# Kernel optimization log

Measured on AMD Instinct MI355X. Metric: run time of the kernel, lower is better.

The kernel has to match this reference:

```python
import jax, jax.numpy as jnp
from jax import lax
import numpy as np

B, C_IN, C_OUT, H, W = 16, 64, 64, 160, 160
K, STRIDE, PAD, DIL, SHIFT = 3, 1, 1, 1, 1


def setup_inputs() -> dict:
    key = jax.random.key(0)
    kx, kw = jax.random.split(key)
    x = jax.random.normal(kx, (B, C_IN, H, W), dtype=jnp.float32)
    weight = jax.random.normal(kw, (C_OUT, C_IN, K, K), dtype=jnp.float32)
    return {"x": x, "weight": weight}


def reference(x, weight):
    Bn, C, Hh, Ww = x.shape
    # zero-pad spatially by shift_distance on all sides (matches F.pad)
    xp = jnp.pad(x, ((0, 0), (0, 0), (SHIFT, SHIFT), (SHIFT, SHIFT)))
    Hp, Wp = Hh + 2 * SHIFT, Ww + 2 * SHIFT
    # shifts list: (dx, dy) for channel groups c % 5
    dxs = jnp.array([0, SHIFT, 0, -SHIFT, 0])
    dys = jnp.array([0, 0, SHIFT, 0, -SHIFT])
    cmod = jnp.arange(C) % 5
    dy = dys[cmod]  # [C] roll along H (dim 2)
    dx = dxs[cmod]  # [C] roll along W (dim 3)
    # torch.roll semantics: out[h, w] = in[(h - dy) % Hp, (w - dx) % Wp]
    row = (jnp.arange(Hp)[None, :] - dy[:, None]) % Hp  # [C, Hp]
    col = (jnp.arange(Wp)[None, :] - dx[:, None]) % Wp  # [C, Wp]
    # single fused gather over channel-dependent row/col indices
    x_shifted = xp[:, jnp.arange(C)[:, None, None], row[:, :, None], col[:, None, :]]
    out = lax.conv_general_dilated(
        x_shifted, weight,
        window_strides=(STRIDE, STRIDE),
        padding=((PAD, PAD), (PAD, PAD)),
        rhs_dilation=(DIL, DIL),
        dimension_numbers=("NCHW", "OIHW", "NCHW"),
    )
    # crop the extra border introduced by the pre-pad
    return out[:, :, 1:-1, 1:-1]
```

## Files before the change

### kernel.cpp

```cpp
#include <hip/hip_runtime.h>
#include <hip/hip_bf16.h>

#define BATCH 16
#define CIN 64
#define COUT 64
#define HH 160
#define WW 160
#define HP 162
#define WP 162

#define ABUF 21760

typedef __attribute__((ext_vector_type(8))) __bf16 bf16x8;
typedef __attribute__((ext_vector_type(4))) float f32x4;
typedef __attribute__((ext_vector_type(8))) unsigned short ushort8;

typedef __attribute__((address_space(1))) const unsigned int gu32;
typedef __attribute__((address_space(3))) unsigned int lu32;

__global__ __launch_bounds__(256) void prep(const float* __restrict__ x,
                                            const float* __restrict__ w,
                                            unsigned short* __restrict__ xs,
                                            unsigned short* __restrict__ wb) {
  __shared__ float lds[64 * 160];

  if (blockIdx.x >= BATCH * HP) {
    int e = (blockIdx.x - BATCH * HP) * 256 + threadIdx.x;
    if (e < 9 * 64 * 64) {
      int tap = e >> 12;
      int o = (e >> 6) & 63;
      int c = e & 63;
      float v = w[((size_t)(o * 64 + c)) * 9 + tap];
      __hip_bfloat16 h = __float2bfloat16(v);
      wb[e] = *reinterpret_cast<unsigned short*>(&h);
    }
    return;
  }

  int y = blockIdx.x % HP;
  int b = blockIdx.x / HP;
  int tid = threadIdx.x;

#pragma unroll
  for (int it = 0; it < 10; ++it) {
    int idx = it * 256 + tid;
    int c = idx / 40;
    int j = idx - c * 40;
    int cm = c % 5;
    int dx = (cm == 1) ? 1 : ((cm == 3) ? -1 : 0);
    int dy = (cm == 2) ? 1 : ((cm == 4) ? -1 : 0);
    int yy = y - dy;
    f32x4 v = {0.f, 0.f, 0.f, 0.f};
    if (yy >= 1 && yy <= HH)
      v = *reinterpret_cast<const f32x4*>(
          x + (((size_t)(b * CIN + c)) * HH + (size_t)(yy - 1)) * WW + j * 4);
    int rot = (c & 31) + dx;
    if (rot < 0) rot += 160;
    int p0 = 4 * j + rot;
#pragma unroll
    for (int e = 0; e < 4; ++e) {
      int p = p0 + e;
      if (p >= 160) p -= 160;
      lds[c * 160 + p] = v[e];
    }
  }
  __syncthreads();

  int cg = tid & 7;
  int xr = tid >> 3;
  int dxe[8], rote[8], rowb[8];
#pragma unroll
  for (int e = 0; e < 8; ++e) {
    int c = cg * 8 + e;
    int cm = c % 5;
    int dx = (cm == 1) ? 1 : ((cm == 3) ? -1 : 0);
    int rot = (c & 31) + dx;
    if (rot < 0) rot += 160;
    dxe[e] = dx;
    rote[e] = rot;
    rowb[e] = c * 160;
  }
  size_t obase = ((size_t)(b * HP + y) * WP) * CIN + cg * 8;
#pragma unroll
  for (int it = 0; it < 6; ++it) {
    int xi = it * 32 + xr;
    if (xi < WP) {
      ushort8 val;
#pragma unroll
      for (int e = 0; e < 8; ++e) {
        int xx = xi - dxe[e] - 1;
        float v = 0.f;
        if (xx >= 0 && xx < WW) {
          int p = rote[e] + xx;
          if (p >= 160) p -= 160;
          v = lds[rowb[e] + p];
        }
        __hip_bfloat16 h = __float2bfloat16(v);
        val[e] = *reinterpret_cast<unsigned short*>(&h);
      }
      *reinterpret_cast<ushort8*>(xs + obase + (size_t)xi * CIN) = val;
    }
  }
}

__global__ __launch_bounds__(256, 1) void conv_mfma(const unsigned short* __restrict__ xs,
                                                    const unsigned short* __restrict__ wb,
                                                    float* __restrict__ out) {
  __shared__ __align__(16) unsigned short lds_a[ABUF];
  __shared__ __align__(16) unsigned short lds_b[ABUF];
  __shared__ __align__(16) unsigned short lds_w[9 * 64 * 64];

  int tid = threadIdx.x;
  int blk = blockIdx.x;
  int tile0 = (blk & 7) * 32 + (blk >> 3);
  int ntiles = (tile0 < 64) ? 7 : 6;

  int wv = tid >> 6;
  int lane = tid & 63;
  int l15 = lane & 15;
  int q = lane >> 4;

  int goff[11];
#pragma unroll
  for (int r = 0; r < 11; ++r) {
    int u = r * 256 + tid;
    int p = u >> 3;
    int j = (u & 7) ^ (p & 7);
    int pr = p / 34, pc = p - pr * 34;
    goff[r] = (pr * WP + pc) * CIN + j * 8;
  }

  int bw0 = l15 * 64 + ((q ^ (l15 & 7)) * 8);
  int bw1 = l15 * 64 + (((4 + q) ^ (l15 & 7)) * 8);

#define STAGE_TO(BUFARR, T_)                                                   \
  {                                                                            \
    int sb_ = (T_) / 100;                                                      \
    int srr_ = (T_) - sb_ * 100;                                               \
    int sti_ = srr_ / 5, stj_ = srr_ - sti_ * 5;                               \
    const unsigned short* srcb_ = xs +                                         \
        ((size_t)sb_ * HP + (size_t)(sti_ * 8)) * WP * CIN +                   \
        (size_t)(stj_ * 32) * CIN;                                             \
    unsigned short* dst0_ = (BUFARR) + wv * 512;                               \
    _Pragma("unroll") for (int r = 0; r < 10; ++r)                             \
        __builtin_amdgcn_global_load_lds((gu32*)(srcb_ + goff[r]),             \
                                         (lu32*)(dst0_ + r * 2048), 16, 0, 0); \
    if (tid < 160)                                                             \
      __builtin_amdgcn_global_load_lds((gu32*)(srcb_ + goff[10]),              \
                                       (lu32*)(dst0_ + 10 * 2048), 16, 0, 0);  \
  }

#define LOAD_A(RBUF, bufp, tt)                                                 \
  {                                                                            \
    const int ch_ = (tt) / 9, ky_ = ((tt) % 9) / 3, kx_ = (tt) % 3;            \
    _Pragma("unroll") for (int mt = 0; mt < 4; ++mt) {                         \
      int pix = 2 * wv * 34 + l15 +                                            \
                (((mt >> 1) + ky_) * 34 + kx_ + (mt & 1) * 16);                \
      int chunk = (ch_ * 4 + q) ^ (pix & 7);                                   \
      Ab[bufp][mt] =                                                           \
          *reinterpret_cast<const bf16x8*>(&(RBUF)[pix * 64 + chunk * 8]);     \
    }                                                                          \
  }

#define LOAD_BW(bufp, tt)                                                      \
  {                                                                            \
    const int ch_ = (tt) / 9, tap_ = (tt) % 9;                                 \
    _Pragma("unroll") for (int nt = 0; nt < 4; ++nt)                           \
        Bb[bufp][nt] = *reinterpret_cast<const bf16x8*>(                       \
            &lds_w[tap_ * 4096 + nt * 1024 + (ch_ ? bw1 : bw0)]);              \
  }

#define TILE_BODY(I_, RBUF, WBUF)                                              \
  {                                                                            \
    int t_ = tile0 + 256 * (I_);                                               \
    int b_ = t_ / 100;                                                         \
    int rr_ = t_ - b_ * 100;                                                   \
    int ti_ = rr_ / 5, tj_ = rr_ - ti_ * 5;                                    \
    int y0_ = ti_ * 8, x0_ = tj_ * 32;                                         \
    if ((I_) + 1 < ntiles) STAGE_TO(WBUF, tile0 + 256 * ((I_) + 1));           \
    _Pragma("unroll") for (int a_ = 0; a_ < 4; ++a_)                           \
      _Pragma("unroll") for (int c2_ = 0; c2_ < 4; ++c2_)                      \
        acc[a_][c2_] = (f32x4){0.f, 0.f, 0.f, 0.f};                            \
    LOAD_A(RBUF, 0, 0);                                                        \
    LOAD_BW(0, 0);                                                             \
    _Pragma("unroll") for (int tt = 0; tt < 18; ++tt) {                        \
      if (tt + 1 < 18) {                                                       \
        LOAD_A(RBUF, (tt + 1) & 1, tt + 1);                                    \
        LOAD_BW((tt + 1) & 1, tt + 1);                                         \
      }                                                                        \
      _Pragma("unroll") for (int mt = 0; mt < 4; ++mt)                         \
        _Pragma("unroll") for (int nt = 0; nt < 4; ++nt)                       \
          acc[mt][nt] = __builtin_amdgcn_mfma_f32_16x16x32_bf16(               \
              Ab[tt & 1][mt], Bb[tt & 1][nt], acc[mt][nt], 0, 0, 0);           \
    }                                                                          \
    __syncthreads();                                                           \
    _Pragma("unroll") for (int mt = 0; mt < 4; ++mt) {                         \
      int orow_ = y0_ + 2 * wv + (mt >> 1);                                    \
      int xo_ = x0_ + (mt & 1) * 16 + q * 4;                                   \
      _Pragma("unroll") for (int nt = 0; nt < 4; ++nt) {                       \
        int o_ = nt * 16 + l15;                                                \
        *reinterpret_cast<f32x4*>(                                             \
            out + ((size_t)(b_ * COUT + o_) * HH + (size_t)orow_) * WW + xo_) = \
            acc[mt][nt];                                                       \
      }                                                                        \
    }                                                                          \
  }

  f32x4 acc[4][4];
  bf16x8 Ab[2][4];
  bf16x8 Bb[2][4];

  for (int r = 0; r < 18; ++r) {
    int u = r * 256 + tid;
    int orow = u >> 3;
    int jj = (u & 7) ^ (orow & 7);
    __builtin_amdgcn_global_load_lds((gu32*)(wb + orow * 64 + jj * 8),
                                     (lu32*)(lds_w + (u & ~63) * 8), 16, 0, 0);
  }
  STAGE_TO(lds_a, tile0);
  __syncthreads();

  for (int i = 0; i < ntiles; i += 2) {
    TILE_BODY(i, lds_a, lds_b);
    if (i + 1 < ntiles) TILE_BODY(i + 1, lds_b, lds_a);
  }

#undef TILE_BODY
#undef LOAD_BW
#undef LOAD_A
#undef STAGE_TO
}

extern "C" void kernel_launch(void* const* d_in, const int* in_sizes, int n_in,
                              void* d_out, int out_size, void* d_ws, size_t ws_size,
                              hipStream_t stream) {
  const float* x = (const float*)d_in[0];
  const float* w = (const float*)d_in[1];
  float* out = (float*)d_out;

  unsigned short* xs = (unsigned short*)d_ws;
  unsigned short* wb = (unsigned short*)((char*)d_ws + (size_t)BATCH * HP * WP * CIN * 2);

  hipLaunchKernelGGL(prep, dim3(BATCH * HP + 144), dim3(256), 0, stream, x, w, xs, wb);
  hipLaunchKernelGGL(conv_mfma, dim3(256), dim3(256), 0, stream, xs, wb, out);
}
```

Measured before the change: 226.5 us.

## Split conv work across eight waves and simplify shift-staging LDS layout

The conv kernel moves from 256 to 512 threads per block. Each of the eight waves now computes one output row (2 M-tiles) instead of two rows (4 M-tiles), and the staging and weight-load loops are re-indexed to match. s_setprio is raised around the MFMA bursts. The aim is more waves in flight per CU to hide LDS and global latency, at the cost of each wave re-reading the full B fragments, which adds LDS read traffic per MFMA. Separately, the prep kernel drops the rotated LDS placement in favour of a plain row stride of 161 floats, which removes the wraparound index arithmetic while still staggering banks.

After: 232.0 us. +2.4%, slower.

```diff
diff --git a/kernel.cpp b/kernel.cpp
--- a/kernel.cpp
+++ b/kernel.cpp
@@ -10,6 +10,7 @@
 #define WP 162
 
 #define ABUF 21760
+#define PSTR 161
 
 typedef __attribute__((ext_vector_type(8))) __bf16 bf16x8;
 typedef __attribute__((ext_vector_type(4))) float f32x4;
@@ -22,7 +23,7 @@
                                             const float* __restrict__ w,
                                             unsigned short* __restrict__ xs,
                                             unsigned short* __restrict__ wb) {
-  __shared__ float lds[64 * 160];
+  __shared__ float lds[64 * PSTR];
 
   if (blockIdx.x >= BATCH * HP) {
     int e = (blockIdx.x - BATCH * HP) * 256 + threadIdx.x;
@@ -47,38 +48,27 @@
     int c = idx / 40;
     int j = idx - c * 40;
     int cm = c % 5;
-    int dx = (cm == 1) ? 1 : ((cm == 3) ? -1 : 0);
     int dy = (cm == 2) ? 1 : ((cm == 4) ? -1 : 0);
     int yy = y - dy;
     f32x4 v = {0.f, 0.f, 0.f, 0.f};
     if (yy >= 1 && yy <= HH)
       v = *reinterpret_cast<const f32x4*>(
           x + (((size_t)(b * CIN + c)) * HH + (size_t)(yy - 1)) * WW + j * 4);
-    int rot = (c & 31) + dx;
-    if (rot < 0) rot += 160;
-    int p0 = 4 * j + rot;
-#pragma unroll
-    for (int e = 0; e < 4; ++e) {
-      int p = p0 + e;
-      if (p >= 160) p -= 160;
-      lds[c * 160 + p] = v[e];
-    }
+    int p0 = c * PSTR + 4 * j;
+#pragma unroll
+    for (int e = 0; e < 4; ++e) lds[p0 + e] = v[e];
   }
   __syncthreads();
 
   int cg = tid & 7;
   int xr = tid >> 3;
-  int dxe[8], rote[8], rowb[8];
+  int dxe[8], rowb[8];
 #pragma unroll
   for (int e = 0; e < 8; ++e) {
     int c = cg * 8 + e;
     int cm = c % 5;
-    int dx = (cm == 1) ? 1 : ((cm == 3) ? -1 : 0);
-    int rot = (c & 31) + dx;
-    if (rot < 0) rot += 160;
-    dxe[e] = dx;
-    rote[e] = rot;
-    rowb[e] = c * 160;
+    dxe[e] = (cm == 1) ? 1 : ((cm == 3) ? -1 : 0);
+    rowb[e] = c * PSTR;
   }
   size_t obase = ((size_t)(b * HP + y) * WP) * CIN + cg * 8;
 #pragma unroll
@@ -90,11 +80,7 @@
       for (int e = 0; e < 8; ++e) {
         int xx = xi - dxe[e] - 1;
         float v = 0.f;
-        if (xx >= 0 && xx < WW) {
-          int p = rote[e] + xx;
-          if (p >= 160) p -= 160;
-          v = lds[rowb[e] + p];
-        }
+        if (xx >= 0 && xx < WW) v = lds[rowb[e] + xx];
         __hip_bfloat16 h = __float2bfloat16(v);
         val[e] = *reinterpret_cast<unsigned short*>(&h);
       }
@@ -103,7 +89,7 @@
   }
 }
 
-__global__ __launch_bounds__(256, 1) void conv_mfma(const unsigned short* __restrict__ xs,
+__global__ __launch_bounds__(512, 1) void conv_mfma(const unsigned short* __restrict__ xs,
                                                     const unsigned short* __restrict__ wb,
                                                     float* __restrict__ out) {
   __shared__ __align__(16) unsigned short lds_a[ABUF];
@@ -120,10 +106,10 @@
   int l15 = lane & 15;
   int q = lane >> 4;
 
-  int goff[11];
-#pragma unroll
-  for (int r = 0; r < 11; ++r) {
-    int u = r * 256 + tid;
+  int goff[6];
+#pragma unroll
+  for (int r = 0; r < 6; ++r) {
+    int u = r * 512 + tid;
     int p = u >> 3;
     int j = (u & 7) ^ (p & 7);
     int pr = p / 34, pc = p - pr * 34;
@@ -142,20 +128,19 @@
         ((size_t)sb_ * HP + (size_t)(sti_ * 8)) * WP * CIN +                   \
         (size_t)(stj_ * 32) * CIN;                                             \
     unsigned short* dst0_ = (BUFARR) + wv * 512;                               \
-    _Pragma("unroll") for (int r = 0; r < 10; ++r)                             \
+    _Pragma("unroll") for (int r = 0; r < 5; ++r)                              \
         __builtin_amdgcn_global_load_lds((gu32*)(srcb_ + goff[r]),             \
-                                         (lu32*)(dst0_ + r * 2048), 16, 0, 0); \
+                                         (lu32*)(dst0_ + r * 4096), 16, 0, 0); \
     if (tid < 160)                                                             \
-      __builtin_amdgcn_global_load_lds((gu32*)(srcb_ + goff[10]),              \
-                                       (lu32*)(dst0_ + 10 * 2048), 16, 0, 0);  \
+      __builtin_amdgcn_global_load_lds((gu32*)(srcb_ + goff[5]),               \
+                                       (lu32*)(dst0_ + 5 * 4096), 16, 0, 0);   \
   }
 
 #define LOAD_A(RBUF, bufp, tt)                                                 \
   {                                                                            \
     const int ch_ = (tt) / 9, ky_ = ((tt) % 9) / 3, kx_ = (tt) % 3;            \
-    _Pragma("unroll") for (int mt = 0; mt < 4; ++mt) {                         \
-      int pix = 2 * wv * 34 + l15 +                                            \
-                (((mt >> 1) + ky_) * 34 + kx_ + (mt & 1) * 16);                \
+    _Pragma("unroll") for (int mt = 0; mt < 2; ++mt) {                         \
+      int pix = (wv + ky_) * 34 + kx_ + l15 + mt * 16;                         \
       int chunk = (ch_ * 4 + q) ^ (pix & 7);                                   \
       Ab[bufp][mt] =                                                           \
           *reinterpret_cast<const bf16x8*>(&(RBUF)[pix * 64 + chunk * 8]);     \
@@ -178,7 +163,7 @@
     int ti_ = rr_ / 5, tj_ = rr_ - ti_ * 5;                                    \
     int y0_ = ti_ * 8, x0_ = tj_ * 32;                                         \
     if ((I_) + 1 < ntiles) STAGE_TO(WBUF, tile0 + 256 * ((I_) + 1));           \
-    _Pragma("unroll") for (int a_ = 0; a_ < 4; ++a_)                           \
+    _Pragma("unroll") for (int a_ = 0; a_ < 2; ++a_)                           \
       _Pragma("unroll") for (int c2_ = 0; c2_ < 4; ++c2_)                      \
         acc[a_][c2_] = (f32x4){0.f, 0.f, 0.f, 0.f};                            \
     LOAD_A(RBUF, 0, 0);                                                        \
@@ -188,15 +173,17 @@
         LOAD_A(RBUF, (tt + 1) & 1, tt + 1);                                    \
         LOAD_BW((tt + 1) & 1, tt + 1);                                         \
       }                                                                        \
-      _Pragma("unroll") for (int mt = 0; mt < 4; ++mt)                         \
+      __builtin_amdgcn_s_setprio(1);                                           \
+      _Pragma("unroll") for (int mt = 0; mt < 2; ++mt)                         \
         _Pragma("unroll") for (int nt = 0; nt < 4; ++nt)                       \
           acc[mt][nt] = __builtin_amdgcn_mfma_f32_16x16x32_bf16(               \
               Ab[tt & 1][mt], Bb[tt & 1][nt], acc[mt][nt], 0, 0, 0);           \
+      __builtin_amdgcn_s_setprio(0);                                           \
     }                                                                          \
     __syncthreads();                                                           \
-    _Pragma("unroll") for (int mt = 0; mt < 4; ++mt) {                         \
-      int orow_ = y0_ + 2 * wv + (mt >> 1);                                    \
-      int xo_ = x0_ + (mt & 1) * 16 + q * 4;                                   \
+    _Pragma("unroll") for (int mt = 0; mt < 2; ++mt) {                         \
+      int orow_ = y0_ + wv;                                                    \
+      int xo_ = x0_ + mt * 16 + q * 4;                                         \
       _Pragma("unroll") for (int nt = 0; nt < 4; ++nt) {                       \
         int o_ = nt * 16 + l15;                                                \
         *reinterpret_cast<f32x4*>(                                             \
@@ -206,12 +193,13 @@
     }                                                                          \
   }
 
-  f32x4 acc[4][4];
-  bf16x8 Ab[2][4];
+  f32x4 acc[2][4];
+  bf16x8 Ab[2][2];
   bf16x8 Bb[2][4];
 
-  for (int r = 0; r < 18; ++r) {
-    int u = r * 256 + tid;
+#pragma unroll
+  for (int r = 0; r < 9; ++r) {
+    int u = r * 512 + tid;
     int orow = u >> 3;
     int jj = (u & 7) ^ (orow & 7);
     __builtin_amdgcn_global_load_lds((gu32*)(wb + orow * 64 + jj * 8),
@@ -242,5 +230,5 @@
   unsigned short* wb = (unsigned short*)((char*)d_ws + (size_t)BATCH * HP * WP * CIN * 2);
 
   hipLaunchKernelGGL(prep, dim3(BATCH * HP + 144), dim3(256), 0, stream, x, w, xs, wb);
-  hipLaunchKernelGGL(conv_mfma, dim3(256), dim3(256), 0, stream, xs, wb, out);
+  hipLaunchKernelGGL(conv_mfma, dim3(256), dim3(512), 0, stream, xs, wb, out);
 }
```
